# Performance work log

Measured on AMD Instinct MI355X. Metric: run time of the kernel, lower is better.

## Reference

```python
import jax, jax.numpy as jnp
import numpy as np

SEQ, B, IN, H = 1024, 64, 512, 512


def drelu(x):
    # optfn drelu: split last dim in half, relu(a) - relu(b) -> halves width
    a, b = jnp.split(x, 2, axis=-1)
    return jax.nn.relu(a) - jax.nn.relu(b)


def setup_inputs() -> dict:
    key = jax.random.key(0)
    k1, k2, k3 = jax.random.split(key, 3)
    inp = jax.random.normal(k1, (SEQ, B, IN), dtype=jnp.float32)
    # Linear weights stored [out_features, in_features] like torch
    W0 = jax.random.normal(k2, (H, H + IN), dtype=jnp.float32) * 0.03
    b0 = jnp.zeros((H,), dtype=jnp.float32)
    W1 = jax.random.normal(k3, (4 * H, H), dtype=jnp.float32) * 0.03
    b1 = jnp.zeros((4 * H,), dtype=jnp.float32)
    return {"input": inp, "W0": W0, "b0": b0, "W1": W1, "b1": b1}


def reference(input, W0, b0, W1, b1):
    hidden = W0.shape[0]
    c0 = jnp.zeros((input.shape[1], hidden), dtype=input.dtype)

    def step(c, x_t):
        x = jnp.concatenate([x_t, c], axis=1)          # [B, IN+H]
        h = jax.nn.relu(x @ W0.T + b0)                 # [B, H]
        y = h @ W1.T + b1                              # [B, 4H]
        new_cx = y[:, : 2 * hidden]                    # [B, 2H]
        new_hx = y[:, 2 * hidden : 3 * hidden]         # [B, H]
        forget = jax.nn.sigmoid(y[:, 3 * hidden :])    # [B, H]
        retain = 1.0 - forget
        new_hx = jax.nn.relu(new_hx)
        new_cx = drelu(new_cx)                         # [B, H]
        c_new = (1.0 - retain) * new_cx + retain * c
        return c_new, new_hx

    c_final, outputs = jax.lax.scan(step, c0, input)
    return outputs, c_final[None]
```

## Files before the change

kernel.cpp:

```cpp
#include <hip/hip_runtime.h>
#include <math.h>

#define SEQ 1024
#define BB  64
#define INF 512
#define HH  512
#define W0LD 1024
#define TSLICE 32768

__global__ __launch_bounds__(256) void xw0_gemm(
    const float* __restrict__ x, const float* __restrict__ W0,
    float* __restrict__ xw)
{
    const int bid = blockIdx.x;
    const int t   = bid >> 3;
    const int jt  = bid & 7;
    const int tid = threadIdx.x;

    __shared__ float xs[64][68];
    __shared__ float ws[64][68];

    const int bq = tid & 15;
    const int jq = tid >> 4;
    float acc[4][4];
    #pragma unroll
    for (int i = 0; i < 4; ++i)
        #pragma unroll
        for (int k = 0; k < 4; ++k) acc[i][k] = 0.f;

    const int r = tid >> 2, q = tid & 3;
    const float* xrow = x  + (size_t)t * BB * INF + (size_t)r * INF;
    const float* wrow = W0 + (size_t)(jt * 64 + r) * W0LD;

    for (int kc = 0; kc < 512; kc += 64) {
        #pragma unroll
        for (int u = 0; u < 4; ++u) {
            const int k0 = 4 * q + 16 * u;
            float4 xv = *reinterpret_cast<const float4*>(xrow + kc + k0);
            xs[k0 + 0][r] = xv.x; xs[k0 + 1][r] = xv.y;
            xs[k0 + 2][r] = xv.z; xs[k0 + 3][r] = xv.w;
            float4 wv = *reinterpret_cast<const float4*>(wrow + kc + k0);
            ws[k0 + 0][r] = wv.x; ws[k0 + 1][r] = wv.y;
            ws[k0 + 2][r] = wv.z; ws[k0 + 3][r] = wv.w;
        }
        __syncthreads();
        #pragma unroll 16
        for (int k = 0; k < 64; ++k) {
            const float4 xv = *reinterpret_cast<const float4*>(&xs[k][bq * 4]);
            const float4 wv = *reinterpret_cast<const float4*>(&ws[k][jq * 4]);
            const float xa[4] = {xv.x, xv.y, xv.z, xv.w};
            const float wa[4] = {wv.x, wv.y, wv.z, wv.w};
            #pragma unroll
            for (int jj = 0; jj < 4; ++jj)
                #pragma unroll
                for (int bb = 0; bb < 4; ++bb)
                    acc[jj][bb] += wa[jj] * xa[bb];
        }
        __syncthreads();
    }

    float* dst = xw + (size_t)t * TSLICE;
    #pragma unroll
    for (int jj = 0; jj < 4; ++jj) {
        const int j = jt * 64 + jq * 4 + jj;
        float4 v = make_float4(acc[jj][0], acc[jj][1], acc[jj][2], acc[jj][3]);
        *reinterpret_cast<float4*>(dst + (size_t)j * 64 + bq * 4) = v;
    }
}

__global__ __launch_bounds__(256) void step1(
    const float* __restrict__ W0, const float* __restrict__ b0,
    const float* __restrict__ cT, const float* __restrict__ xw,
    float* __restrict__ hT, int t)
{
    const int jt  = blockIdx.x;
    const int tid = threadIdx.x;
    const int b   = tid & 63;
    const int jl  = (tid >> 6) & 1;
    const int kh  = tid >> 7;
    const int j   = jt * 2 + jl;

    const int woff = __builtin_amdgcn_readfirstlane(j * W0LD + INF + kh * 256);
    const float* __restrict__ wrow = W0 + woff;
    const float* __restrict__ cp   = cT + kh * 256 * 64 + b;

    float acc = 0.f;
    #pragma unroll 8
    for (int k = 0; k < 256; k += 4) {
        const float4 w4 = *reinterpret_cast<const float4*>(wrow + k);
        acc += cp[(k + 0) * 64] * w4.x + cp[(k + 1) * 64] * w4.y +
               cp[(k + 2) * 64] * w4.z + cp[(k + 3) * 64] * w4.w;
    }

    __shared__ float red[128];
    if (kh == 1) red[jl * 64 + b] = acc;
    __syncthreads();
    if (kh == 0) {
        const float tot = acc + red[jl * 64 + b] + b0[j] +
                          xw[(size_t)t * TSLICE + (size_t)j * 64 + b];
        hT[j * 64 + b] = fmaxf(tot, 0.f);
    }
}

__global__ __launch_bounds__(256) void step2(
    const float* __restrict__ W1, const float* __restrict__ b1,
    const float* __restrict__ hT, float* __restrict__ cT,
    float* __restrict__ out, int t)
{
    const int jt  = blockIdx.x;
    const int tid = threadIdx.x;
    const int b   = tid & 63;
    const int jl  = (tid >> 6) & 1;
    const int gh  = tid >> 7;
    const int j   = jt * 2 + jl;
    const int g0  = gh * 2, g1 = g0 + 1;

    const int r0 = __builtin_amdgcn_readfirstlane((g0 * HH + j) * HH);
    const int r1 = __builtin_amdgcn_readfirstlane((g1 * HH + j) * HH);
    const float* __restrict__ w0p = W1 + r0;
    const float* __restrict__ w1p = W1 + r1;
    const float* __restrict__ hp  = hT + b;

    float a0 = 0.f, a1 = 0.f;
    #pragma unroll 8
    for (int k = 0; k < 512; k += 4) {
        const float4 u = *reinterpret_cast<const float4*>(w0p + k);
        const float4 v = *reinterpret_cast<const float4*>(w1p + k);
        const float h0 = hp[(k + 0) * 64], h1 = hp[(k + 1) * 64];
        const float h2 = hp[(k + 2) * 64], h3 = hp[(k + 3) * 64];
        a0 += h0 * u.x + h1 * u.y + h2 * u.z + h3 * u.w;
        a1 += h0 * v.x + h1 * v.y + h2 * v.z + h3 * v.w;
    }
    a0 += b1[g0 * HH + j];
    a1 += b1[g1 * HH + j];

    __shared__ float red[2][64][2];
    if (gh == 1) { red[jl][b][0] = a0; red[jl][b][1] = a1; }
    __syncthreads();
    if (gh == 0) {
        const float yh  = red[jl][b][0];
        const float yf  = red[jl][b][1];
        const float ncx = fmaxf(a0, 0.f) - fmaxf(a1, 0.f);
        const float f   = 1.f / (1.f + expf(-yf));
        const int   idx = j * 64 + b;
        const float cn  = f * ncx + (1.f - f) * cT[idx];
        cT[idx] = cn;
        out[(size_t)t * TSLICE + (size_t)b * HH + j] = fmaxf(yh, 0.f);
        if (t == SEQ - 1)
            out[(size_t)SEQ * TSLICE + (size_t)b * HH + j] = cn;
    }
}

extern "C" void kernel_launch(void* const* d_in, const int* in_sizes, int n_in,
                              void* d_out, int out_size, void* d_ws, size_t ws_size,
                              hipStream_t stream)
{
    const float* x  = (const float*)d_in[0];
    const float* W0 = (const float*)d_in[1];
    const float* b0 = (const float*)d_in[2];
    const float* W1 = (const float*)d_in[3];
    const float* b1 = (const float*)d_in[4];

    float* out = (float*)d_out;
    float* cT  = (float*)d_ws;
    float* hT  = cT + (size_t)HH * BB;

    hipMemsetAsync(cT, 0, (size_t)HH * BB * sizeof(float), stream);

    xw0_gemm<<<8192, 256, 0, stream>>>(x, W0, out);

    for (int t = 0; t < SEQ; ++t) {
        step1<<<256, 256, 0, stream>>>(W0, b0, cT, out, hT, t);
        step2<<<256, 256, 0, stream>>>(W1, b1, hT, cT, out, t);
    }
}
```

Baseline: 23.28 ms.

## Replace per-step kernel launches with a persistent kernel using grid barriers

```diff
diff --git a/kernel.cpp b/kernel.cpp
--- a/kernel.cpp
+++ b/kernel.cpp
@@ -7,6 +7,7 @@
 #define HH  512
 #define W0LD 1024
 #define TSLICE 32768
+#define NWG 256
 
 __global__ __launch_bounds__(256) void xw0_gemm(
     const float* __restrict__ x, const float* __restrict__ W0,
@@ -68,86 +69,113 @@
     }
 }
 
-__global__ __launch_bounds__(256) void step1(
+__device__ __forceinline__ void gbar(int* cnt, int* gen)
+{
+    asm volatile("s_waitcnt vmcnt(0)" ::: "memory");
+    __syncthreads();
+    if (threadIdx.x == 0) {
+        __threadfence();
+        int g = __hip_atomic_load(gen, __ATOMIC_RELAXED, __HIP_MEMORY_SCOPE_AGENT);
+        int a = __hip_atomic_fetch_add(cnt, 1, __ATOMIC_RELAXED, __HIP_MEMORY_SCOPE_AGENT);
+        if (a == NWG - 1) {
+            __hip_atomic_store(cnt, 0, __ATOMIC_RELAXED, __HIP_MEMORY_SCOPE_AGENT);
+            __hip_atomic_store(gen, g + 1, __ATOMIC_RELEASE, __HIP_MEMORY_SCOPE_AGENT);
+        } else {
+            while (__hip_atomic_load(gen, __ATOMIC_RELAXED, __HIP_MEMORY_SCOPE_AGENT) == g)
+                __builtin_amdgcn_s_sleep(2);
+        }
+        __threadfence();
+    }
+    __syncthreads();
+}
+
+__global__ __launch_bounds__(256) void dlstm_persist(
     const float* __restrict__ W0, const float* __restrict__ b0,
-    const float* __restrict__ cT, const float* __restrict__ xw,
-    float* __restrict__ hT, int t)
-{
-    const int jt  = blockIdx.x;
+    const float* __restrict__ W1, const float* __restrict__ b1,
+    float* __restrict__ out, float* __restrict__ cT, float* __restrict__ hT,
+    int* __restrict__ bcnt, int* __restrict__ bgen)
+{
+    const int wg  = blockIdx.x;
     const int tid = threadIdx.x;
     const int b   = tid & 63;
     const int jl  = (tid >> 6) & 1;
     const int kh  = tid >> 7;
-    const int j   = jt * 2 + jl;
-
-    const int woff = __builtin_amdgcn_readfirstlane(j * W0LD + INF + kh * 256);
-    const float* __restrict__ wrow = W0 + woff;
-    const float* __restrict__ cp   = cT + kh * 256 * 64 + b;
-
-    float acc = 0.f;
-    #pragma unroll 8
-    for (int k = 0; k < 256; k += 4) {
-        const float4 w4 = *reinterpret_cast<const float4*>(wrow + k);
-        acc += cp[(k + 0) * 64] * w4.x + cp[(k + 1) * 64] * w4.y +
-               cp[(k + 2) * 64] * w4.z + cp[(k + 3) * 64] * w4.w;
-    }
-
-    __shared__ float red[128];
-    if (kh == 1) red[jl * 64 + b] = acc;
+    const int j   = wg * 2 + jl;
+
+    __shared__ float wA[2][512];
+    __shared__ float wB[2][2][512][2];
+    __shared__ float redA[2][64];
+    __shared__ float redB[2][64][2];
+
+    for (int i = tid; i < 2 * 512; i += 256) {
+        const int sjl = i >> 9, k = i & 511;
+        wA[sjl][k] = W0[(size_t)(wg * 2 + sjl) * W0LD + INF + k];
+    }
+    for (int i = tid; i < 4096; i += 256) {
+        const int p   = i & 1;
+        const int k   = (i >> 1) & 511;
+        const int sgh = (i >> 10) & 1;
+        const int sjl = (i >> 11) & 1;
+        wB[sjl][sgh][k][p] =
+            W1[(size_t)((2 * sgh + p) * HH + wg * 2 + sjl) * HH + k];
+    }
+    const float b0j = b0[j];
+    const float b1a = b1[(2 * kh + 0) * HH + j];
+    const float b1b = b1[(2 * kh + 1) * HH + j];
     __syncthreads();
-    if (kh == 0) {
-        const float tot = acc + red[jl * 64 + b] + b0[j] +
-                          xw[(size_t)t * TSLICE + (size_t)j * 64 + b];
-        hT[j * 64 + b] = fmaxf(tot, 0.f);
-    }
-}
-
-__global__ __launch_bounds__(256) void step2(
-    const float* __restrict__ W1, const float* __restrict__ b1,
-    const float* __restrict__ hT, float* __restrict__ cT,
-    float* __restrict__ out, int t)
-{
-    const int jt  = blockIdx.x;
-    const int tid = threadIdx.x;
-    const int b   = tid & 63;
-    const int jl  = (tid >> 6) & 1;
-    const int gh  = tid >> 7;
-    const int j   = jt * 2 + jl;
-    const int g0  = gh * 2, g1 = g0 + 1;
-
-    const int r0 = __builtin_amdgcn_readfirstlane((g0 * HH + j) * HH);
-    const int r1 = __builtin_amdgcn_readfirstlane((g1 * HH + j) * HH);
-    const float* __restrict__ w0p = W1 + r0;
-    const float* __restrict__ w1p = W1 + r1;
-    const float* __restrict__ hp  = hT + b;
-
-    float a0 = 0.f, a1 = 0.f;
-    #pragma unroll 8
-    for (int k = 0; k < 512; k += 4) {
-        const float4 u = *reinterpret_cast<const float4*>(w0p + k);
-        const float4 v = *reinterpret_cast<const float4*>(w1p + k);
-        const float h0 = hp[(k + 0) * 64], h1 = hp[(k + 1) * 64];
-        const float h2 = hp[(k + 2) * 64], h3 = hp[(k + 3) * 64];
-        a0 += h0 * u.x + h1 * u.y + h2 * u.z + h3 * u.w;
-        a1 += h0 * v.x + h1 * v.y + h2 * v.z + h3 * v.w;
-    }
-    a0 += b1[g0 * HH + j];
-    a1 += b1[g1 * HH + j];
-
-    __shared__ float red[2][64][2];
-    if (gh == 1) { red[jl][b][0] = a0; red[jl][b][1] = a1; }
-    __syncthreads();
-    if (gh == 0) {
-        const float yh  = red[jl][b][0];
-        const float yf  = red[jl][b][1];
-        const float ncx = fmaxf(a0, 0.f) - fmaxf(a1, 0.f);
-        const float f   = 1.f / (1.f + expf(-yf));
-        const int   idx = j * 64 + b;
-        const float cn  = f * ncx + (1.f - f) * cT[idx];
-        cT[idx] = cn;
-        out[(size_t)t * TSLICE + (size_t)b * HH + j] = fmaxf(yh, 0.f);
-        if (t == SEQ - 1)
-            out[(size_t)SEQ * TSLICE + (size_t)b * HH + j] = cn;
+
+    const float* __restrict__ xwp = out + (size_t)j * 64 + b;
+    const int jj64b = j * 64 + b;
+
+    for (int t = 0; t < SEQ; ++t) {
+        {
+            const float* __restrict__ cp = cT + (kh << 8) * 64 + b;
+            const float* __restrict__ wa = &wA[jl][kh << 8];
+            float acc = 0.f;
+            #pragma unroll 8
+            for (int k = 0; k < 256; k += 4) {
+                const float4 w = *reinterpret_cast<const float4*>(wa + k);
+                acc += cp[(k + 0) * 64] * w.x + cp[(k + 1) * 64] * w.y +
+                       cp[(k + 2) * 64] * w.z + cp[(k + 3) * 64] * w.w;
+            }
+            if (kh == 1) redA[jl][b] = acc;
+            __syncthreads();
+            if (kh == 0) {
+                const float tot = acc + redA[jl][b] + b0j + xwp[(size_t)t * TSLICE];
+                hT[jj64b] = fmaxf(tot, 0.f);
+            }
+        }
+        gbar(bcnt, bgen);
+
+        {
+            const float* __restrict__ hp = hT + b;
+            const float* __restrict__ wb = &wB[jl][kh][0][0];
+            float a0 = 0.f, a1 = 0.f;
+            #pragma unroll 8
+            for (int k = 0; k < 512; k += 2) {
+                const float4 w = *reinterpret_cast<const float4*>(wb + 2 * k);
+                const float h0 = hp[(k + 0) * 64];
+                const float h1 = hp[(k + 1) * 64];
+                a0 += h0 * w.x + h1 * w.z;
+                a1 += h0 * w.y + h1 * w.w;
+            }
+            a0 += b1a;
+            a1 += b1b;
+            if (kh == 1) { redB[jl][b][0] = a0; redB[jl][b][1] = a1; }
+            __syncthreads();
+            if (kh == 0) {
+                const float yh  = redB[jl][b][0];
+                const float yf  = redB[jl][b][1];
+                const float ncx = fmaxf(a0, 0.f) - fmaxf(a1, 0.f);
+                const float f   = 1.f / (1.f + expf(-yf));
+                const float cn  = f * ncx + (1.f - f) * cT[jj64b];
+                cT[jj64b] = cn;
+                out[(size_t)t * TSLICE + (size_t)b * HH + j] = fmaxf(yh, 0.f);
+                if (t == SEQ - 1)
+                    out[(size_t)SEQ * TSLICE + (size_t)b * HH + j] = cn;
+            }
+        }
+        gbar(bcnt, bgen);
     }
 }
 
@@ -162,15 +190,16 @@
     const float* b1 = (const float*)d_in[4];
 
     float* out = (float*)d_out;
-    float* cT  = (float*)d_ws;
-    float* hT  = cT + (size_t)HH * BB;
-
-    hipMemsetAsync(cT, 0, (size_t)HH * BB * sizeof(float), stream);
+
+    int*   bcnt = (int*)d_ws;
+    int*   bgen = bcnt + 1;
+    float* cT   = (float*)((char*)d_ws + 1024);
+    float* hT   = cT + (size_t)HH * BB;
+
+    hipMemsetAsync(d_ws, 0, 1024 + (size_t)HH * BB * sizeof(float), stream);
 
     xw0_gemm<<<8192, 256, 0, stream>>>(x, W0, out);
 
-    for (int t = 0; t < SEQ; ++t) {
-        step1<<<256, 256, 0, stream>>>(W0, b0, cT, out, hT, t);
-        step2<<<256, 256, 0, stream>>>(W1, b1, hT, cT, out, t);
-    }
-}
+    dlstm_persist<<<NWG, 256, 0, stream>>>(W0, b0, W1, b1, out, cT, hT,
+                                           bcnt, bgen);
+}
```

Measured after the change: 62.56 ms. 169% more time.
